# Performance work log

Measured on AMD Instinct MI355X. Metric: run time of the kernel, lower is better.

## Reference

```python
import jax, jax.numpy as jnp
import numpy as np

MARGIN = 0.3
NEG_FILL = -100.0
EPS = 1e-6


def setup_inputs() -> dict:
    key = jax.random.key(0)
    k1, k2, k3 = jax.random.split(key, 3)
    B, N, D = 256, 131072, 128
    xembs = jax.random.normal(k1, (B, D), dtype=jnp.float32)
    yembs = jax.random.normal(k2, (N, D), dtype=jnp.float32)
    pos_inds = jax.random.randint(k3, (B, 1), 0, N, dtype=jnp.int64)
    # target: multi-hot label matrix; positives marked 1 at pos_inds
    target = jnp.zeros((B, N), dtype=jnp.float32)
    target = target.at[jnp.arange(B)[:, None], pos_inds].set(1.0)
    return {"xembs": xembs, "yembs": yembs, "target": target,
            "pos_inds": pos_inds, "num_neg": 5}


def reference(xembs, yembs, target, pos_inds, num_neg):
    # sim: [B, N]
    sim = xembs @ yembs.T
    # positive similarities: [B, 1]
    sim_p = jnp.take_along_axis(sim, pos_inds, axis=1)
    # mask out positives, mine hardest negatives
    neg_sim = jnp.where(target < EPS, sim, NEG_FILL)
    _, idx = jax.lax.top_k(neg_sim, num_neg)          # [B, num_neg]
    sim_n = jnp.take_along_axis(sim, idx, axis=1)      # [B, num_neg]
    # hinge triplet loss
    loss = jnp.maximum(jnp.zeros_like(sim_n), sim_n - sim_p + MARGIN)
    mask = (loss != 0).astype(loss.dtype)
    prob = jax.nn.softmax(sim_n * mask, axis=1)
    return (loss * prob).mean()
```

## Files before the change

kernel.cpp:

```cpp
#include <hip/hip_runtime.h>

#define BROWS 256
#define NCOLS 131072
#define DDIM  128
#define K     5
#define MARGIN 0.3f

#define NBLK  512
#define CPB   (NCOLS / NBLK)
#define NIT   (CPB / 16)
#define ZGATE 3.4f
#define CAP   128
#define YSTR  68

typedef __attribute__((ext_vector_type(8))) __bf16 bf16x8;
typedef __attribute__((ext_vector_type(4))) float f32x4;
typedef __attribute__((ext_vector_type(4))) unsigned int u32x4;

__device__ __forceinline__ unsigned pack_bf16(float a, float b) {
    unsigned ua = __float_as_uint(a), ub = __float_as_uint(b);
    unsigned ra = (ua + 0x7fffu + ((ua >> 16) & 1u)) >> 16;
    unsigned rb = (ub + 0x7fffu + ((ub >> 16) & 1u)) & 0xffff0000u;
    return ra | rb;
}

__device__ __forceinline__ u32x4 pack8(const float4& a, const float4& b) {
    u32x4 t;
    t[0] = pack_bf16(a.x, a.y); t[1] = pack_bf16(a.z, a.w);
    t[2] = pack_bf16(b.x, b.y); t[3] = pack_bf16(b.z, b.w);
    return t;
}

__global__ __launch_bounds__(256) void init_kernel(
    const float* __restrict__ x, float* __restrict__ thr,
    int* __restrict__ cnt, float* __restrict__ out)
{
    const int t = threadIdx.x;
    const float* xp = x + (size_t)t * DDIM;
    float s = 0.f;
#pragma unroll
    for (int k = 0; k < DDIM; k += 4) {
        const float4 v = *(const float4*)(xp + k);
        s = fmaf(v.x, v.x, s); s = fmaf(v.y, v.y, s);
        s = fmaf(v.z, v.z, s); s = fmaf(v.w, v.w, s);
    }
    thr[t] = ZGATE * sqrtf(s);
    cnt[t] = 0;
    if (t == 0) out[0] = 0.f;
}

__global__ __launch_bounds__(256, 2) void gemm_collect_kernel(
    const float* __restrict__ x, const float* __restrict__ y,
    const float* __restrict__ thr,
    int* __restrict__ cnt, float* __restrict__ bufv, int* __restrict__ bufc)
{
    __shared__ unsigned ybf[2][16 * YSTR];

    const int tid   = threadIdx.x;
    const int lane  = tid & 63;
    const int quad  = lane >> 4;
    const int l15   = lane & 15;
    const int wrow0 = tid & 192;
    const int col0  = blockIdx.x * CPB;

    bf16x8 af[4][4];
#pragma unroll
    for (int mt = 0; mt < 4; ++mt) {
        const float* xp = x + (size_t)(wrow0 + mt * 16 + l15) * DDIM + quad * 8;
#pragma unroll
        for (int s = 0; s < 4; ++s) {
            const float4 a = *(const float4*)(xp + s * 32);
            const float4 b = *(const float4*)(xp + s * 32 + 4);
            const u32x4 t = pack8(a, b);
            af[mt][s] = __builtin_bit_cast(bf16x8, t);
        }
    }

    float thrv[16];
#pragma unroll
    for (int mt = 0; mt < 4; ++mt)
#pragma unroll
        for (int r = 0; r < 4; ++r)
            thrv[mt * 4 + r] = thr[wrow0 + mt * 16 + quad * 4 + r];

    const int sc = tid >> 4, sj = tid & 15;
    const float* ysrc = y + (size_t)(col0 + sc) * DDIM + sj * 8;
    const unsigned sdst = sc * YSTR + sj * 4;
    const unsigned frag_off = l15 * YSTR + quad * 4;

    float4 ga = *(const float4*)(ysrc);
    float4 gb = *(const float4*)(ysrc + 4);
    *(u32x4*)(&ybf[0][0] + sdst) = pack8(ga, gb);

    for (int it = 0; it < NIT; ++it) {
        if (it + 1 < NIT) {
            const float* yn = ysrc + (size_t)(it + 1) * 16 * DDIM;
            ga = *(const float4*)(yn);
            gb = *(const float4*)(yn + 4);
        }
        __syncthreads();

        const unsigned* yb = &ybf[it & 1][0];
        bf16x8 bfrag[4];
#pragma unroll
        for (int s = 0; s < 4; ++s)
            bfrag[s] = __builtin_bit_cast(bf16x8, *(const u32x4*)(yb + frag_off + s * 16));

        f32x4 acc[4];
#pragma unroll
        for (int mt = 0; mt < 4; ++mt) acc[mt] = (f32x4){0.f, 0.f, 0.f, 0.f};
#pragma unroll
        for (int s = 0; s < 4; ++s)
#pragma unroll
            for (int mt = 0; mt < 4; ++mt)
                acc[mt] = __builtin_amdgcn_mfma_f32_16x16x32_bf16(af[mt][s], bfrag[s], acc[mt], 0, 0, 0);

        if (it + 1 < NIT)
            *(u32x4*)(&ybf[(it + 1) & 1][0] + sdst) = pack8(ga, gb);

        float m = -1.f;
#pragma unroll
        for (int mt = 0; mt < 4; ++mt)
#pragma unroll
            for (int r = 0; r < 4; ++r)
                m = fmaxf(m, acc[mt][r] - thrv[mt * 4 + r]);
        if (m > 0.f) {
            const int col = col0 + it * 16 + l15;
#pragma unroll
            for (int mt = 0; mt < 4; ++mt)
#pragma unroll
                for (int r = 0; r < 4; ++r) {
                    const float v = acc[mt][r];
                    if (v > thrv[mt * 4 + r]) {
                        const int row = wrow0 + mt * 16 + quad * 4 + r;
                        const int idx = atomicAdd(&cnt[row], 1);
                        if (idx < CAP) {
                            bufv[row * CAP + idx] = v;
                            bufc[row * CAP + idx] = col;
                        }
                    }
                }
        }
    }
}

__device__ __forceinline__ void insert5(float* t5, float v) {
    if (v > t5[K - 1]) {
        float nv = v;
#pragma unroll
        for (int p = 0; p < K; ++p) {
            const bool gt = nv > t5[p];
            const float tv = t5[p];
            if (gt) { t5[p] = nv; nv = tv; }
        }
    }
}

__device__ __forceinline__ void merge5(float* __restrict__ t5, const float* __restrict__ src) {
#pragma unroll
    for (int p = 0; p < K; ++p) insert5(t5, src[p]);
}

__device__ __forceinline__ float epilogue(const float* t5, float sp) {
    float loss[K], logit[K];
#pragma unroll
    for (int p = 0; p < K; ++p) {
        loss[p]  = fmaxf(0.f, t5[p] - sp + MARGIN);
        logit[p] = (loss[p] != 0.f) ? t5[p] : 0.f;
    }
    float mx = logit[0];
#pragma unroll
    for (int p = 1; p < K; ++p) mx = fmaxf(mx, logit[p]);
    float den = 0.f, num = 0.f;
#pragma unroll
    for (int p = 0; p < K; ++p) {
        const float e = __expf(logit[p] - mx);
        den += e;
        num += loss[p] * e;
    }
    return num / den;
}

__global__ __launch_bounds__(256) void reduce_kernel(
    const float* __restrict__ x, const float* __restrict__ y,
    const int* __restrict__ pos, const int* __restrict__ cnt,
    const float* __restrict__ bufv, const int* __restrict__ bufc,
    int* __restrict__ flag, float* __restrict__ out)
{
    const int row = blockIdx.x;
    const int tid = threadIdx.x;
    __shared__ float sred[256];
    __shared__ float sv[256 * K];

    const int prow = pos[row];
    float p = 0.f;
    if (tid < DDIM) p = x[row * DDIM + tid] * y[(size_t)prow * DDIM + tid];
    sred[tid] = p;
    __syncthreads();
    for (int s = 128; s >= 1; s >>= 1) {
        if (tid < s) sred[tid] += sred[tid + s];
        __syncthreads();
    }

    const int c = cnt[row];
    const int n = c < CAP ? c : CAP;
    float t5[K];
#pragma unroll
    for (int q = 0; q < K; ++q) t5[q] = -3.0e38f;
    if (tid < n && bufc[row * CAP + tid] != prow)
        t5[0] = bufv[row * CAP + tid];

#pragma unroll
    for (int q = 0; q < K; ++q) sv[tid * K + q] = t5[q];
    __syncthreads();
    for (int s = 128; s >= 1; s >>= 1) {
        if (tid < s) {
            merge5(t5, &sv[(tid + s) * K]);
#pragma unroll
            for (int q = 0; q < K; ++q) sv[tid * K + q] = t5[q];
        }
        __syncthreads();
    }

    if (tid == 0) {
        const bool ok = (c <= CAP) && (t5[K - 1] > -1.0e38f);
        flag[row] = ok ? 0 : 1;
        if (ok) atomicAdd(out, epilogue(t5, sred[0]) * (1.0f / (BROWS * K)));
    }
}

__global__ __launch_bounds__(256) void fallback_kernel(
    const float* __restrict__ x, const float* __restrict__ y,
    const int* __restrict__ pos, const int* __restrict__ flag,
    float* __restrict__ out)
{
    const int row = blockIdx.x;
    if (flag[row] == 0) return;
    const int tid = threadIdx.x;
    const int prow = pos[row];
    __shared__ float xr[DDIM];
    __shared__ float sv[256 * K];
    if (tid < DDIM) xr[tid] = x[row * DDIM + tid];
    __syncthreads();

    float t5[K];
#pragma unroll
    for (int q = 0; q < K; ++q) t5[q] = -3.0e38f;
    for (int col = tid; col < NCOLS; col += 256) {
        if (col == prow) continue;
        const float* yp = y + (size_t)col * DDIM;
        float d = 0.f;
        for (int k = 0; k < DDIM; ++k) d = fmaf(xr[k], yp[k], d);
        insert5(t5, d);
    }
#pragma unroll
    for (int q = 0; q < K; ++q) sv[tid * K + q] = t5[q];
    __syncthreads();
    for (int s = 128; s >= 1; s >>= 1) {
        if (tid < s) {
            merge5(t5, &sv[(tid + s) * K]);
#pragma unroll
            for (int q = 0; q < K; ++q) sv[tid * K + q] = t5[q];
        }
        __syncthreads();
    }
    if (tid == 0) {
        float sp = 0.f;
        const float* yp = y + (size_t)prow * DDIM;
        for (int k = 0; k < DDIM; ++k) sp = fmaf(xr[k], yp[k], sp);
        atomicAdd(out, epilogue(t5, sp) * (1.0f / (BROWS * K)));
    }
}

extern "C" void kernel_launch(void* const* d_in, const int* in_sizes, int n_in,
                              void* d_out, int out_size, void* d_ws, size_t ws_size,
                              hipStream_t stream) {
    const float* x  = (const float*)d_in[0];
    const float* y  = (const float*)d_in[1];
    const int* pos  = (const int*)d_in[3];

    int*   cnt  = (int*)d_ws;
    int*   flag = cnt + BROWS;
    float* thr  = (float*)(flag + BROWS);
    float* bufv = thr + BROWS;
    int*   bufc = (int*)(bufv + (size_t)BROWS * CAP);

    init_kernel<<<dim3(1), 256, 0, stream>>>(x, thr, cnt, (float*)d_out);
    gemm_collect_kernel<<<dim3(NBLK), 256, 0, stream>>>(x, y, thr, cnt, bufv, bufc);
    reduce_kernel<<<dim3(BROWS), 256, 0, stream>>>(x, y, pos, cnt, bufv, bufc, flag, (float*)d_out);
    fallback_kernel<<<dim3(BROWS), 256, 0, stream>>>(x, y, pos, flag, (float*)d_out);
}
```

Measured before the change: 237.3 us.

## Widen column tile, deepen y prefetch, fuse threshold and fallback kernels

The GEMM tile grows from 16 to 32 columns per iteration, with y loads prefetched two iterations ahead in registers to hide global latency and halve the number of barriers. Bf16 packing now uses the hardware v_cvt_pk_bf16_f32 instruction instead of integer rounding. The per-row threshold is computed inside each GEMM block, which is redundant work across blocks but removes a dependency on init_kernel. The fallback path is merged into reduce_kernel, dropping one kernel launch and the flag array. The cost is higher register pressure from the doubled accumulators and prefetch buffers.

```diff
diff --git a/kernel.cpp b/kernel.cpp
--- a/kernel.cpp
+++ b/kernel.cpp
@@ -8,7 +8,8 @@
 
 #define NBLK  512
 #define CPB   (NCOLS / NBLK)
-#define NIT   (CPB / 16)
+#define TCOLS 32
+#define NIT   (CPB / TCOLS)
 #define ZGATE 3.4f
 #define CAP   128
 #define YSTR  68
@@ -18,10 +19,9 @@
 typedef __attribute__((ext_vector_type(4))) unsigned int u32x4;
 
 __device__ __forceinline__ unsigned pack_bf16(float a, float b) {
-    unsigned ua = __float_as_uint(a), ub = __float_as_uint(b);
-    unsigned ra = (ua + 0x7fffu + ((ua >> 16) & 1u)) >> 16;
-    unsigned rb = (ub + 0x7fffu + ((ub >> 16) & 1u)) & 0xffff0000u;
-    return ra | rb;
+    unsigned r;
+    asm("v_cvt_pk_bf16_f32 %0, %1, %2" : "=v"(r) : "v"(a), "v"(b));
+    return r;
 }
 
 __device__ __forceinline__ u32x4 pack8(const float4& a, const float4& b) {
@@ -32,29 +32,19 @@
 }
 
 __global__ __launch_bounds__(256) void init_kernel(
-    const float* __restrict__ x, float* __restrict__ thr,
     int* __restrict__ cnt, float* __restrict__ out)
 {
     const int t = threadIdx.x;
-    const float* xp = x + (size_t)t * DDIM;
-    float s = 0.f;
-#pragma unroll
-    for (int k = 0; k < DDIM; k += 4) {
-        const float4 v = *(const float4*)(xp + k);
-        s = fmaf(v.x, v.x, s); s = fmaf(v.y, v.y, s);
-        s = fmaf(v.z, v.z, s); s = fmaf(v.w, v.w, s);
-    }
-    thr[t] = ZGATE * sqrtf(s);
     cnt[t] = 0;
     if (t == 0) out[0] = 0.f;
 }
 
 __global__ __launch_bounds__(256, 2) void gemm_collect_kernel(
     const float* __restrict__ x, const float* __restrict__ y,
-    const float* __restrict__ thr,
     int* __restrict__ cnt, float* __restrict__ bufv, int* __restrict__ bufc)
 {
-    __shared__ unsigned ybf[2][16 * YSTR];
+    __shared__ unsigned ybf[2][TCOLS * YSTR];
+    __shared__ float sthr[BROWS];
 
     const int tid   = threadIdx.x;
     const int lane  = tid & 63;
@@ -63,6 +53,18 @@
     const int wrow0 = tid & 192;
     const int col0  = blockIdx.x * CPB;
 
+    {
+        const float* xp = x + (size_t)tid * DDIM;
+        float s = 0.f;
+#pragma unroll
+        for (int k = 0; k < DDIM; k += 4) {
+            const float4 v = *(const float4*)(xp + k);
+            s = fmaf(v.x, v.x, s); s = fmaf(v.y, v.y, s);
+            s = fmaf(v.z, v.z, s); s = fmaf(v.w, v.w, s);
+        }
+        sthr[tid] = ZGATE * sqrtf(s);
+    }
+
     bf16x8 af[4][4];
 #pragma unroll
     for (int mt = 0; mt < 4; ++mt) {
@@ -76,70 +78,97 @@
         }
     }
 
+    const int scol = tid >> 3;
+    const int skk  = tid & 7;
+    const float* ysrc = y + (size_t)(col0 + scol) * DDIM + skk * 16;
+    const unsigned sdst = scol * YSTR + skk * 8;
+    const unsigned frag_off = l15 * YSTR + quad * 4;
+
+    float4 sl[2][4];
+#pragma unroll
+    for (int q = 0; q < 4; ++q) sl[0][q] = *(const float4*)(ysrc + q * 4);
+#pragma unroll
+    for (int q = 0; q < 4; ++q) sl[1][q] = *(const float4*)(ysrc + TCOLS * DDIM + q * 4);
+    {
+        u32x4* d = (u32x4*)(&ybf[0][0] + sdst);
+        d[0] = pack8(sl[0][0], sl[0][1]);
+        d[1] = pack8(sl[0][2], sl[0][3]);
+    }
+    __syncthreads();
+
     float thrv[16];
 #pragma unroll
     for (int mt = 0; mt < 4; ++mt)
 #pragma unroll
         for (int r = 0; r < 4; ++r)
-            thrv[mt * 4 + r] = thr[wrow0 + mt * 16 + quad * 4 + r];
-
-    const int sc = tid >> 4, sj = tid & 15;
-    const float* ysrc = y + (size_t)(col0 + sc) * DDIM + sj * 8;
-    const unsigned sdst = sc * YSTR + sj * 4;
-    const unsigned frag_off = l15 * YSTR + quad * 4;
-
-    float4 ga = *(const float4*)(ysrc);
-    float4 gb = *(const float4*)(ysrc + 4);
-    *(u32x4*)(&ybf[0][0] + sdst) = pack8(ga, gb);
-
+            thrv[mt * 4 + r] = sthr[wrow0 + mt * 16 + quad * 4 + r];
+
+#pragma unroll 2
     for (int it = 0; it < NIT; ++it) {
-        if (it + 1 < NIT) {
-            const float* yn = ysrc + (size_t)(it + 1) * 16 * DDIM;
-            ga = *(const float4*)(yn);
-            gb = *(const float4*)(yn + 4);
-        }
-        __syncthreads();
+        if (it + 2 < NIT) {
+            const float* yn = ysrc + (size_t)(it + 2) * TCOLS * DDIM;
+#pragma unroll
+            for (int q = 0; q < 4; ++q) sl[it & 1][q] = *(const float4*)(yn + q * 4);
+        }
+        if (it) __syncthreads();
 
         const unsigned* yb = &ybf[it & 1][0];
+
+        f32x4 acc[2][4];
         bf16x8 bfrag[4];
 #pragma unroll
         for (int s = 0; s < 4; ++s)
             bfrag[s] = __builtin_bit_cast(bf16x8, *(const u32x4*)(yb + frag_off + s * 16));
-
-        f32x4 acc[4];
-#pragma unroll
-        for (int mt = 0; mt < 4; ++mt) acc[mt] = (f32x4){0.f, 0.f, 0.f, 0.f};
+#pragma unroll
+        for (int mt = 0; mt < 4; ++mt) acc[0][mt] = (f32x4){0.f, 0.f, 0.f, 0.f};
 #pragma unroll
         for (int s = 0; s < 4; ++s)
 #pragma unroll
             for (int mt = 0; mt < 4; ++mt)
-                acc[mt] = __builtin_amdgcn_mfma_f32_16x16x32_bf16(af[mt][s], bfrag[s], acc[mt], 0, 0, 0);
-
-        if (it + 1 < NIT)
-            *(u32x4*)(&ybf[(it + 1) & 1][0] + sdst) = pack8(ga, gb);
-
-        float m = -1.f;
-#pragma unroll
-        for (int mt = 0; mt < 4; ++mt)
-#pragma unroll
-            for (int r = 0; r < 4; ++r)
-                m = fmaxf(m, acc[mt][r] - thrv[mt * 4 + r]);
-        if (m > 0.f) {
-            const int col = col0 + it * 16 + l15;
+                acc[0][mt] = __builtin_amdgcn_mfma_f32_16x16x32_bf16(af[mt][s], bfrag[s], acc[0][mt], 0, 0, 0);
+
+        if (it + 1 < NIT) {
+            u32x4* d = (u32x4*)(&ybf[(it + 1) & 1][0] + sdst);
+            d[0] = pack8(sl[(it + 1) & 1][0], sl[(it + 1) & 1][1]);
+            d[1] = pack8(sl[(it + 1) & 1][2], sl[(it + 1) & 1][3]);
+        }
+
+#pragma unroll
+        for (int s = 0; s < 4; ++s)
+            bfrag[s] = __builtin_bit_cast(bf16x8, *(const u32x4*)(yb + 16 * YSTR + frag_off + s * 16));
+#pragma unroll
+        for (int mt = 0; mt < 4; ++mt) acc[1][mt] = (f32x4){0.f, 0.f, 0.f, 0.f};
+#pragma unroll
+        for (int s = 0; s < 4; ++s)
 #pragma unroll
             for (int mt = 0; mt < 4; ++mt)
-#pragma unroll
-                for (int r = 0; r < 4; ++r) {
-                    const float v = acc[mt][r];
-                    if (v > thrv[mt * 4 + r]) {
-                        const int row = wrow0 + mt * 16 + quad * 4 + r;
-                        const int idx = atomicAdd(&cnt[row], 1);
-                        if (idx < CAP) {
-                            bufv[row * CAP + idx] = v;
-                            bufc[row * CAP + idx] = col;
+                acc[1][mt] = __builtin_amdgcn_mfma_f32_16x16x32_bf16(af[mt][s], bfrag[s], acc[1][mt], 0, 0, 0);
+
+#pragma unroll
+        for (int cg = 0; cg < 2; ++cg) {
+            float m = -1.f;
+#pragma unroll
+            for (int mt = 0; mt < 4; ++mt)
+#pragma unroll
+                for (int r = 0; r < 4; ++r)
+                    m = fmaxf(m, acc[cg][mt][r] - thrv[mt * 4 + r]);
+            if (m > 0.f) {
+                const int col = col0 + it * TCOLS + cg * 16 + l15;
+#pragma unroll
+                for (int mt = 0; mt < 4; ++mt)
+#pragma unroll
+                    for (int r = 0; r < 4; ++r) {
+                        const float v = acc[cg][mt][r];
+                        if (v > thrv[mt * 4 + r]) {
+                            const int row = wrow0 + mt * 16 + quad * 4 + r;
+                            const int idx = atomicAdd(&cnt[row], 1);
+                            if (idx < CAP) {
+                                bufv[row * CAP + idx] = v;
+                                bufc[row * CAP + idx] = col;
+                            }
                         }
                     }
-                }
+            }
         }
     }
 }
@@ -185,12 +214,14 @@
     const float* __restrict__ x, const float* __restrict__ y,
     const int* __restrict__ pos, const int* __restrict__ cnt,
     const float* __restrict__ bufv, const int* __restrict__ bufc,
-    int* __restrict__ flag, float* __restrict__ out)
+    float* __restrict__ out)
 {
     const int row = blockIdx.x;
     const int tid = threadIdx.x;
     __shared__ float sred[256];
     __shared__ float sv[256 * K];
+    __shared__ float xr[DDIM];
+    __shared__ int   sok;
 
     const int prow = pos[row];
     float p = 0.f;
@@ -201,6 +232,7 @@
         if (tid < s) sred[tid] += sred[tid + s];
         __syncthreads();
     }
+    const float sp = sred[0];
 
     const int c = cnt[row];
     const int n = c < CAP ? c : CAP;
@@ -223,27 +255,15 @@
     }
 
     if (tid == 0) {
-        const bool ok = (c <= CAP) && (t5[K - 1] > -1.0e38f);
-        flag[row] = ok ? 0 : 1;
-        if (ok) atomicAdd(out, epilogue(t5, sred[0]) * (1.0f / (BROWS * K)));
-    }
-}
-
-__global__ __launch_bounds__(256) void fallback_kernel(
-    const float* __restrict__ x, const float* __restrict__ y,
-    const int* __restrict__ pos, const int* __restrict__ flag,
-    float* __restrict__ out)
-{
-    const int row = blockIdx.x;
-    if (flag[row] == 0) return;
-    const int tid = threadIdx.x;
-    const int prow = pos[row];
-    __shared__ float xr[DDIM];
-    __shared__ float sv[256 * K];
+        sok = (c <= CAP && t5[K - 1] > -1.0e38f) ? 1 : 0;
+        if (sok) atomicAdd(out, epilogue(t5, sp) * (1.0f / (BROWS * K)));
+    }
+    __syncthreads();
+    if (sok) return;
+
     if (tid < DDIM) xr[tid] = x[row * DDIM + tid];
     __syncthreads();
 
-    float t5[K];
 #pragma unroll
     for (int q = 0; q < K; ++q) t5[q] = -3.0e38f;
     for (int col = tid; col < NCOLS; col += 256) {
@@ -264,12 +284,7 @@
         }
         __syncthreads();
     }
-    if (tid == 0) {
-        float sp = 0.f;
-        const float* yp = y + (size_t)prow * DDIM;
-        for (int k = 0; k < DDIM; ++k) sp = fmaf(xr[k], yp[k], sp);
-        atomicAdd(out, epilogue(t5, sp) * (1.0f / (BROWS * K)));
-    }
+    if (tid == 0) atomicAdd(out, epilogue(t5, sp) * (1.0f / (BROWS * K)));
 }
 
 extern "C" void kernel_launch(void* const* d_in, const int* in_sizes, int n_in,
@@ -280,13 +295,10 @@
     const int* pos  = (const int*)d_in[3];
 
     int*   cnt  = (int*)d_ws;
-    int*   flag = cnt + BROWS;
-    float* thr  = (float*)(flag + BROWS);
-    float* bufv = thr + BROWS;
+    float* bufv = (float*)(cnt + BROWS);
     int*   bufc = (int*)(bufv + (size_t)BROWS * CAP);
 
-    init_kernel<<<dim3(1), 256, 0, stream>>>(x, thr, cnt, (float*)d_out);
-    gemm_collect_kernel<<<dim3(NBLK), 256, 0, stream>>>(x, y, thr, cnt, bufv, bufc);
-    reduce_kernel<<<dim3(BROWS), 256, 0, stream>>>(x, y, pos, cnt, bufv, bufc, flag, (float*)d_out);
-    fallback_kernel<<<dim3(BROWS), 256, 0, stream>>>(x, y, pos, flag, (float*)d_out);
-}
+    init_kernel<<<dim3(1), 256, 0, stream>>>(cnt, (float*)d_out);
+    gemm_collect_kernel<<<dim3(NBLK), 256, 0, stream>>>(x, y, cnt, bufv, bufc);
+    reduce_kernel<<<dim3(BROWS), 256, 0, stream>>>(x, y, pos, cnt, bufv, bufc, (float*)d_out);
+}
```

Measured after the change: 236.3 us. Within noise of the previous version (-0.4%).
